# Kernel tuning notes

Measured on AMD Instinct MI355X. Metric: run time of the kernel, lower is better.

## Reference

```python
import jax, jax.numpy as jnp
import numpy as np
import math

B, L, WIN, D, H, FF, NL, V, M = 16, 2048, 128, 512, 8, 2048, 3, 32000, 32
HD = D // H
EPS = 1e-5
RECON_W = 0.1

def _ln(x, g, b):
    m = x.mean(-1, keepdims=True)
    v = ((x - m) ** 2).mean(-1, keepdims=True)
    return (x - m) * jax.lax.rsqrt(v + EPS) * g + b

def _denoiser(x_t, t, motif, left, right, glob, time_proj_W, time_proj_b, cond_proj_W, cond_proj_b,
              qkv_W, qkv_b, attn_out_W, attn_out_b, ff1_W, ff1_b, ff2_W, ff2_b,
              ln1_g, ln1_b, ln2_g, ln2_b, out_W, out_b):
    half = D // 2
    freqs = jnp.exp(-math.log(10000.0) * jnp.arange(half) / (half - 1))
    a = t[:, None] * freqs[None, :]
    temb = jnp.concatenate([jnp.sin(a), jnp.cos(a)], -1) @ time_proj_W.T + time_proj_b
    x = x_t + temb[:, None, :]
    cond = jnp.concatenate([motif, left, right, glob], -1) @ cond_proj_W.T + cond_proj_b
    x = jnp.concatenate([cond[:, None, :], x], 1)
    S = x.shape[1]
    for i in range(NL):  # post-norm TransformerEncoderLayer, relu, no dropout (eval)
        qkv = x @ qkv_W[i].T + qkv_b[i]
        q, k, v = jnp.split(qkv, 3, axis=-1)
        q = q.reshape(B, S, H, HD); k = k.reshape(B, S, H, HD); v = v.reshape(B, S, H, HD)
        attn = jax.nn.softmax(jnp.einsum('bqhd,bkhd->bhqk', q, k) / math.sqrt(HD), axis=-1)
        ctx = jnp.einsum('bhqk,bkhd->bqhd', attn, v).reshape(B, S, D)
        x = _ln(x + ctx @ attn_out_W[i].T + attn_out_b[i], ln1_g[i], ln1_b[i])
        h = jax.nn.relu(x @ ff1_W[i].T + ff1_b[i]) @ ff2_W[i].T + ff2_b[i]
        x = _ln(x + h, ln2_g[i], ln2_b[i])
    return x[:, 1:, :] @ out_W.T + out_b

def setup_inputs():
    key = jax.random.key(0)
    ks = jax.random.split(key, 20)
    s = 0.02
    inp = {}
    inp['token_ids'] = jax.random.randint(ks[0], (B, L), 0, V)
    inp['motif_ids'] = jax.random.randint(ks[1], (B, M), 0, V)
    inp['motif_len'] = jax.random.randint(ks[2], (B,), 1, M + 1)
    inp['window_start'] = jax.random.randint(ks[3], (B,), 0, L - WIN)
    lens = jax.random.randint(ks[4], (B,), 1, WIN + 1).at[0].set(WIN)
    inp['window_end'] = inp['window_start'] + lens
    inp['t'] = jax.random.uniform(ks[5], (B,))
    inp['x0'] = jax.random.normal(ks[6], (B, WIN, D))
    inp['embed_table'] = jax.random.normal(ks[7], (V, D)) * s
    inp['decode_W'] = jax.random.normal(ks[8], (V, D)) * s
    inp['decode_b'] = jnp.zeros((V,))
    inp['adapter_W'] = jax.random.normal(ks[9], (D, D)) * s
    inp['adapter_b'] = jnp.zeros((D,))
    inp['time_proj_W'] = jax.random.normal(ks[10], (D, D)) * s
    inp['time_proj_b'] = jnp.zeros((D,))
    inp['cond_proj_W'] = jax.random.normal(ks[11], (D, 4 * D)) * s
    inp['cond_proj_b'] = jnp.zeros((D,))
    inp['qkv_W'] = jax.random.normal(ks[12], (NL, 3 * D, D)) * s
    inp['qkv_b'] = jnp.zeros((NL, 3 * D))
    inp['attn_out_W'] = jax.random.normal(ks[13], (NL, D, D)) * s
    inp['attn_out_b'] = jnp.zeros((NL, D))
    inp['ff1_W'] = jax.random.normal(ks[14], (NL, FF, D)) * s
    inp['ff1_b'] = jnp.zeros((NL, FF))
    inp['ff2_W'] = jax.random.normal(ks[15], (NL, D, FF)) * s
    inp['ff2_b'] = jnp.zeros((NL, D))
    inp['ln1_g'] = jnp.ones((NL, D)); inp['ln1_b'] = jnp.zeros((NL, D))
    inp['ln2_g'] = jnp.ones((NL, D)); inp['ln2_b'] = jnp.zeros((NL, D))
    inp['out_W'] = jax.random.normal(ks[16], (D, D)) * s
    inp['out_b'] = jnp.zeros((D,))
    return inp

def _forward(token_ids, motif_ids, motif_len, window_start, window_end, t, x0,
             embed_table, decode_W, decode_b, adapter_W, adapter_b, den):
    hidden = embed_table[token_ids]  # frozen backbone encode: [B, L, D]
    pos = jnp.arange(L)
    def pool(s, e):  # vectorized masked mean over region [s, e)
        m = ((pos[None, :] >= s[:, None]) & (pos[None, :] < e[:, None])).astype(hidden.dtype)
        return jnp.einsum('bl,bld->bd', m, hidden) / jnp.maximum(m.sum(1, keepdims=True), 1.0)
    left = pool(jnp.zeros_like(window_start), window_start)
    right = pool(window_end, jnp.full_like(window_end, L))
    glob = hidden.mean(1)
    memb = embed_table[motif_ids]
    mmask = (jnp.arange(M)[None, :] < motif_len[:, None]).astype(memb.dtype)
    motif = (memb * mmask[..., None]).sum(1) / jnp.maximum(motif_len.astype(memb.dtype), 1.0)[:, None]
    actual = jnp.clip(window_end - window_start, 0, WIN)
    win_mask = jnp.arange(WIN)[None, :] < actual[:, None]
    idx = jnp.clip(window_start[:, None] + jnp.arange(WIN)[None, :], 0, L - 1)
    x1 = jnp.take_along_axis(hidden, idx[:, :, None], axis=1) * win_mask[..., None]
    x_t = (1 - t[:, None, None]) * x0 + t[:, None, None] * x1
    target_v = x1 - x0
    pred_v = _denoiser(x_t, t, motif, left, right, glob, *den)
    valid = win_mask[..., None].astype(x1.dtype)
    vel = (((pred_v - target_v) ** 2) * valid).sum() / (jnp.maximum(valid.sum(), 1.0) * D)
    pred_x1 = x_t + (1 - t[:, None, None]) * pred_v
    logits = (pred_x1 @ adapter_W.T + adapter_b) @ decode_W.T + decode_b
    labels = jnp.where(win_mask, jnp.take_along_axis(token_ids, idx, axis=1), -100)
    lv = labels != -100
    logp = jax.nn.log_softmax(logits, axis=-1)
    picked = jnp.take_along_axis(logp, jnp.maximum(labels, 0)[..., None], axis=-1)[..., 0]
    recon = -(picked * lv).sum() / jnp.maximum(lv.sum(), 1)
    return vel + RECON_W * recon

def reference(token_ids, motif_ids, motif_len, window_start, window_end, t, x0,
              embed_table, decode_W, decode_b, adapter_W, adapter_b,
              time_proj_W, time_proj_b, cond_proj_W, cond_proj_b, qkv_W, qkv_b,
              attn_out_W, attn_out_b, ff1_W, ff1_b, ff2_W, ff2_b,
              ln1_g, ln1_b, ln2_g, ln2_b, out_W, out_b):
    den = (time_proj_W, time_proj_b, cond_proj_W, cond_proj_b, qkv_W, qkv_b,
           attn_out_W, attn_out_b, ff1_W, ff1_b, ff2_W, ff2_b,
           ln1_g, ln1_b, ln2_g, ln2_b, out_W, out_b)
    return _forward(token_ids, motif_ids, motif_len, window_start, window_end, t, x0,
                    embed_table, decode_W, decode_b, adapter_W, adapter_b, den)
```

## Files before the change

kernel.cpp:

```cpp
#include <hip/hip_runtime.h>
#include <hip/hip_bf16.h>
#include <math.h>

typedef __hip_bfloat16 bf16;

constexpr int cB = 16, cL = 2048, cWIN = 128, cD = 512, cH = 8, cFF = 2048;
constexpr int cNL = 3, cV = 32000, cM = 32;
constexpr int cHD = cD / cH;
constexpr int cS = cWIN + 1;
constexpr float cEPS = 1e-5f;
constexpr float cRECON_W = 0.1f;
constexpr int cNVT = cV / 128;

__device__ __forceinline__ float b2f(bf16 x) { return __bfloat162float(x); }

__device__ __forceinline__ float ldx(const void* p, size_t i, int f32) {
    return f32 ? ((const float*)p)[i]
               : __bfloat162float(((const bf16*)p)[i]);
}

__device__ __forceinline__ unsigned int f2bf(float f) {
    union { float f; unsigned int u; } v; v.f = f;
    unsigned int u = v.u + 0x7FFFu + ((v.u >> 16) & 1u);
    return u >> 16;
}

__device__ __forceinline__ void glds16(const unsigned short* g, unsigned short* l) {
    __builtin_amdgcn_global_load_lds(
        (const __attribute__((address_space(1))) void*)g,
        (__attribute__((address_space(3))) void*)l, 16, 0, 0);
}

typedef short bf16x8 __attribute__((ext_vector_type(8)));
typedef float f32x4  __attribute__((ext_vector_type(4)));

__global__ void detect_kernel(const void* __restrict__ x0raw, int* __restrict__ flag)
{
    const unsigned short* h = (const unsigned short*)x0raw;
    int tid = threadIdx.x;
    int cnt = 0;
    for (int j = tid; j < 8192; j += 256) {
        unsigned short u = h[2 * j];
        int e = (u >> 7) & 0xFF;
        if (e >= 134) cnt++;
    }
    __shared__ int red[256];
    red[tid] = cnt; __syncthreads();
    for (int off = 128; off > 0; off >>= 1) {
        if (tid < off) red[tid] += red[tid + off];
        __syncthreads();
    }
    if (tid == 0) *flag = (red[0] > 400) ? 1 : 0;
}

__global__ __launch_bounds__(512) void pools_part_kernel(
    const int* __restrict__ tok, const int* __restrict__ wstart,
    const int* __restrict__ wend, const void* __restrict__ emb,
    float* __restrict__ part, const int* __restrict__ dflag)
{
    const int f32 = *dflag;
    int chunk = blockIdx.x;
    int b = blockIdx.y;
    int d = threadIdx.x;
    int ws_ = wstart[b], we_ = wend[b];
    float sl = 0.f, sr = 0.f, sg = 0.f;
    int l0 = chunk * 128;
    for (int l = l0; l < l0 + 128; ++l) {
        int t = tok[b * cL + l];
        float h = ldx(emb, (size_t)t * cD + d, f32);
        sg += h;
        if (l < ws_) sl += h;
        if (l >= we_) sr += h;
    }
    size_t base = ((size_t)(b * 16 + chunk)) * 3 * cD;
    part[base + d]            = sl;
    part[base + cD + d]       = sr;
    part[base + 2 * cD + d]   = sg;
}

__global__ __launch_bounds__(512) void pools_combine_kernel(
    const float* __restrict__ part, const int* __restrict__ mids,
    const int* __restrict__ mlen, const int* __restrict__ wstart,
    const int* __restrict__ wend, const void* __restrict__ emb,
    unsigned short* __restrict__ featb, const int* __restrict__ dflag)
{
    const int f32 = *dflag;
    int b = blockIdx.x;
    int d = threadIdx.x;
    int ws_ = wstart[b], we_ = wend[b];
    float sl = 0.f, sr = 0.f, sg = 0.f;
    for (int c = 0; c < 16; ++c) {
        size_t base = ((size_t)(b * 16 + c)) * 3 * cD;
        sl += part[base + d];
        sr += part[base + cD + d];
        sg += part[base + 2 * cD + d];
    }
    int ml = mlen[b];
    float sm = 0.f;
    for (int j = 0; j < cM; ++j) {
        if (j < ml) sm += ldx(emb, (size_t)mids[b * cM + j] * cD + d, f32);
    }
    unsigned short* fr = featb + (size_t)b * (4 * cD);
    fr[d]            = (unsigned short)f2bf(sm / fmaxf((float)ml, 1.f));
    fr[cD + d]       = (unsigned short)f2bf(sl / fmaxf((float)ws_, 1.f));
    fr[2 * cD + d]   = (unsigned short)f2bf(sr / fmaxf((float)(cL - we_), 1.f));
    fr[3 * cD + d]   = (unsigned short)f2bf(sg / (float)cL);
}

__global__ __launch_bounds__(512) void tf_kernel(
    const void* __restrict__ t_arr, unsigned short* __restrict__ tfbb,
    const int* __restrict__ dflag)
{
    const int f32 = *dflag;
    int b = blockIdx.x;
    int j = threadIdx.x;
    float t = ldx(t_arr, b, f32);
    const int half = cD / 2;
    float v;
    if (j < half) {
        float fr = expf(-logf(10000.f) * (float)j / (float)(half - 1));
        v = sinf(t * fr);
    } else {
        float fr = expf(-logf(10000.f) * (float)(j - half) / (float)(half - 1));
        v = cosf(t * fr);
    }
    tfbb[(size_t)b * cD + j] = (unsigned short)f2bf(v);
}

__global__ __launch_bounds__(512) void build_x_kernel(
    const int* __restrict__ tok, const int* __restrict__ wstart,
    const int* __restrict__ wend, const void* __restrict__ t_arr,
    const void* __restrict__ x0, const void* __restrict__ emb,
    const float* __restrict__ cond, const float* __restrict__ temb,
    float* __restrict__ x, unsigned short* __restrict__ xbf,
    float* __restrict__ x1, float* __restrict__ xt,
    const int* __restrict__ dflag)
{
    const int f32 = *dflag;
    int row = blockIdx.x;
    int b = row / cS, s = row % cS;
    int d = threadIdx.x;
    if (s == 0) {
        float cv = cond[b * cD + d];
        x[(size_t)row * cD + d] = cv;
        xbf[(size_t)row * cD + d] = (unsigned short)f2bf(cv);
        return;
    }
    int i = s - 1;
    int ws_ = wstart[b], we_ = wend[b];
    int actual = min(max(we_ - ws_, 0), cWIN);
    int idx = min(ws_ + i, cL - 1);
    float x1v = 0.f;
    if (i < actual) x1v = ldx(emb, (size_t)tok[b * cL + idx] * cD + d, f32);
    float t = ldx(t_arr, b, f32);
    float x0v = ldx(x0, ((size_t)b * cWIN + i) * cD + d, f32);
    float xtv = (1.f - t) * x0v + t * x1v;
    size_t ro = ((size_t)b * cWIN + i) * cD + d;
    x1[ro] = x1v;
    xt[ro] = xtv;
    float xv = xtv + temb[b * cD + d];
    x[(size_t)row * cD + d] = xv;
    xbf[(size_t)row * cD + d] = (unsigned short)f2bf(xv);
}

constexpr int GL2 = 72;
__global__ __launch_bounds__(256) void gemm_bf(
    const unsigned short* __restrict__ Abf, const void* __restrict__ Wb,
    size_t wOff, const void* __restrict__ biasb, size_t bOff,
    float* __restrict__ Cf, unsigned short* __restrict__ Cbf,
    int Mdim, int Ndim, int Kdim, int relu, int obf, int amap,
    const int* __restrict__ dflag)
{
    const int f32 = *dflag;
    const float* Wf = (const float*)Wb + wOff;
    const unsigned short* Wh = (const unsigned short*)Wb + wOff;
    __shared__ unsigned short As[2][64 * GL2];
    __shared__ unsigned short Bs[2][64 * GL2];
    const int tid = threadIdx.x;
    const int lane = tid & 63;
    const int wid = tid >> 6;
    const int wm = wid >> 1, wn = wid & 1;
    const int quad = lane >> 4, lm = lane & 15;
    const int m0 = blockIdx.y * 64;
    const int n0 = blockIdx.x * 64;

    f32x4 acc[2][2];
    #pragma unroll
    for (int i = 0; i < 2; ++i)
        #pragma unroll
        for (int j = 0; j < 2; ++j)
            acc[i][j] = (f32x4){0.f, 0.f, 0.f, 0.f};

    const int srow = tid >> 3;
    const int sc8  = (tid & 7) * 8;
    const int ssw  = ((tid & 7) ^ ((tid >> 3) & 7)) * 8;
    const int lmm  = lm & 7;

    auto loadA = [&](int k0, uint4* r) {
        #pragma unroll
        for (int t = 0; t < 2; ++t) {
            int r0 = m0 + srow + t * 32;
            uint4 v = {0u, 0u, 0u, 0u};
            if (r0 < Mdim) {
                size_t ar = amap ? ((size_t)(r0 >> 7) * cS + 1 + (r0 & 127))
                                 : (size_t)r0;
                v = *(const uint4*)(Abf + ar * Kdim + k0 + sc8);
            }
            r[t] = v;
        }
    };
    auto loadB = [&](int k0, uint4* r) {
        #pragma unroll
        for (int t = 0; t < 2; ++t) {
            int row = srow + t * 32;
            size_t g = (size_t)(n0 + row) * Kdim + k0 + sc8;
            if (f32) {
                float4 v0 = *(const float4*)(Wf + g);
                float4 v1 = *(const float4*)(Wf + g + 4);
                r[t] = make_uint4(
                    f2bf(v0.x) | (f2bf(v0.y) << 16), f2bf(v0.z) | (f2bf(v0.w) << 16),
                    f2bf(v1.x) | (f2bf(v1.y) << 16), f2bf(v1.z) | (f2bf(v1.w) << 16));
            } else {
                r[t] = *(const uint4*)(Wh + g);
            }
        }
    };
    auto stores = [&](int buf, const uint4* ra, const uint4* rb) {
        #pragma unroll
        for (int u = 0; u < 2; ++u) {
            *(uint4*)(&As[buf][(srow + u * 32) * GL2 + ssw]) = ra[u];
            *(uint4*)(&Bs[buf][(srow + u * 32) * GL2 + ssw]) = rb[u];
        }
    };
    auto compute = [&](int buf) {
        #pragma unroll
        for (int kk = 0; kk < 2; ++kk) {
            const int sl = ((kk * 4 + quad) ^ lmm) * 8;
            bf16x8 a0 = *(const bf16x8*)(&As[buf][(wm * 32 + lm) * GL2 + sl]);
            bf16x8 a1 = *(const bf16x8*)(&As[buf][(wm * 32 + 16 + lm) * GL2 + sl]);
            bf16x8 b0 = *(const bf16x8*)(&Bs[buf][(wn * 32 + lm) * GL2 + sl]);
            bf16x8 b1 = *(const bf16x8*)(&Bs[buf][(wn * 32 + 16 + lm) * GL2 + sl]);
            acc[0][0] = __builtin_amdgcn_mfma_f32_16x16x32_bf16(a0, b0, acc[0][0], 0, 0, 0);
            acc[0][1] = __builtin_amdgcn_mfma_f32_16x16x32_bf16(a0, b1, acc[0][1], 0, 0, 0);
            acc[1][0] = __builtin_amdgcn_mfma_f32_16x16x32_bf16(a1, b0, acc[1][0], 0, 0, 0);
            acc[1][1] = __builtin_amdgcn_mfma_f32_16x16x32_bf16(a1, b1, acc[1][1], 0, 0, 0);
        }
    };

    uint4 raA[2], rbA[2], raB[2], rbB[2];
    loadA(0, raA);  loadB(0, rbA);
    loadA(64, raB); loadB(64, rbB);
    const int nk = Kdim >> 6;
    for (int t = 0; t < nk; t += 2) {
        stores(0, raA, rbA);
        __syncthreads();
        if (t + 2 < nk) { loadA((t + 2) * 64, raA); loadB((t + 2) * 64, rbA); }
        compute(0);
        stores(1, raB, rbB);
        __syncthreads();
        if (t + 3 < nk) { loadA((t + 3) * 64, raB); loadB((t + 3) * 64, rbB); }
        compute(1);
    }

    #pragma unroll
    for (int in = 0; in < 2; ++in) {
        int gc = n0 + wn * 32 + in * 16 + lm;
        float bv = ldx(biasb, bOff + gc, f32);
        #pragma unroll
        for (int im = 0; im < 2; ++im) {
            #pragma unroll
            for (int r = 0; r < 4; ++r) {
                int gr = m0 + wm * 32 + im * 16 + quad * 4 + r;
                if (gr < Mdim) {
                    float v = acc[im][in][r] + bv;
                    if (relu) v = fmaxf(v, 0.f);
                    if (obf) Cbf[(size_t)gr * Ndim + gc] = (unsigned short)f2bf(v);
                    else     Cf[(size_t)gr * Ndim + gc] = v;
                }
            }
        }
    }
}

__global__ __launch_bounds__(256) void attn_mfma_kernel(
    const unsigned short* __restrict__ qkv, unsigned short* __restrict__ ctx)
{
    constexpr int SP = 160;
    constexpr int KP = 72;
    constexpr int VP = 168;
    const int h = blockIdx.x, b = blockIdx.y, z = blockIdx.z;
    const int tid = threadIdx.x;
    const int lane = tid & 63;
    const int wid = tid >> 6;
    const int quad = lane >> 4, lm = lane & 15;

    __shared__ unsigned short Ks[SP * KP];
    __shared__ unsigned short Vt[64 * VP];
    __shared__ unsigned short Pl[4 * 16 * VP];

    const unsigned short* base = qkv + (size_t)b * cS * (3 * cD) + h * cHD;

    for (int c = tid; c < SP * 8; c += 256) {
        int row = c >> 3, g = c & 7;
        uint4 v = {0u, 0u, 0u, 0u};
        if (row < cS)
            v = *(const uint4*)(base + (size_t)row * (3 * cD) + cD + g * 8);
        *(uint4*)(Ks + row * KP + g * 8) = v;
    }
    for (int c = tid; c < SP * 16; c += 256) {
        int key = c >> 4, d4 = c & 15;
        uint2 v = {0u, 0u};
        if (key < cS)
            v = *(const uint2*)(base + (size_t)key * (3 * cD) + 2 * cD + d4 * 4);
        Vt[(d4 * 4 + 0) * VP + key] = (unsigned short)(v.x & 0xFFFFu);
        Vt[(d4 * 4 + 1) * VP + key] = (unsigned short)(v.x >> 16);
        Vt[(d4 * 4 + 2) * VP + key] = (unsigned short)(v.y & 0xFFFFu);
        Vt[(d4 * 4 + 3) * VP + key] = (unsigned short)(v.y >> 16);
    }
    __syncthreads();

    unsigned short* Pw = Pl + wid * (16 * VP);
    const int t = z * 3 + wid;

    if (wid < 3 && t < 9) {
        int qs = t * 16 + lm;
        bf16x8 aq[2];
        #pragma unroll
        for (int j = 0; j < 8; ++j) { aq[0][j] = 0; aq[1][j] = 0; }
        if (qs < cS) {
            const unsigned short* qrow = base + (size_t)qs * (3 * cD);
            aq[0] = *(const bf16x8*)(qrow + quad * 8);
            aq[1] = *(const bf16x8*)(qrow + 32 + quad * 8);
        }

        f32x4 sc[10];
        #pragma unroll
        for (int n = 0; n < 10; ++n) {
            sc[n] = (f32x4){0.f, 0.f, 0.f, 0.f};
            bf16x8 bk0 = *(const bf16x8*)(Ks + (n * 16 + lm) * KP + quad * 8);
            sc[n] = __builtin_amdgcn_mfma_f32_16x16x32_bf16(aq[0], bk0, sc[n], 0, 0, 0);
            bf16x8 bk1 = *(const bf16x8*)(Ks + (n * 16 + lm) * KP + 32 + quad * 8);
            sc[n] = __builtin_amdgcn_mfma_f32_16x16x32_bf16(aq[1], bk1, sc[n], 0, 0, 0);
        }

        #pragma unroll
        for (int r = 0; r < 4; ++r) {
            float mx = -3.0e38f;
            #pragma unroll
            for (int n = 0; n < 10; ++n) {
                float v = sc[n][r] * 0.125f;
                mx = fmaxf(mx, ((n * 16 + lm) < cS) ? v : -3.0e38f);
            }
            #pragma unroll
            for (int msk = 1; msk < 16; msk <<= 1)
                mx = fmaxf(mx, __shfl_xor(mx, msk));
            float p[10];
            float sum = 0.f;
            #pragma unroll
            for (int n = 0; n < 10; ++n) {
                float e = ((n * 16 + lm) < cS) ? expf(sc[n][r] * 0.125f - mx) : 0.f;
                p[n] = e; sum += e;
            }
            #pragma unroll
            for (int msk = 1; msk < 16; msk <<= 1)
                sum += __shfl_xor(sum, msk);
            float inv = 1.f / sum;
            unsigned short* pr = Pw + (quad * 4 + r) * VP + lm;
            #pragma unroll
            for (int n = 0; n < 10; ++n)
                pr[n * 16] = (unsigned short)f2bf(p[n] * inv);
        }

        asm volatile("s_waitcnt lgkmcnt(0)" ::: "memory");
        __builtin_amdgcn_sched_barrier(0);

        f32x4 o[4];
        #pragma unroll
        for (int j = 0; j < 4; ++j) o[j] = (f32x4){0.f, 0.f, 0.f, 0.f};
        #pragma unroll
        for (int ks = 0; ks < 5; ++ks) {
            bf16x8 ap = *(const bf16x8*)(Pw + lm * VP + ks * 32 + quad * 8);
            #pragma unroll
            for (int j = 0; j < 4; ++j) {
                bf16x8 bv = *(const bf16x8*)(Vt + (j * 16 + lm) * VP + ks * 32 + quad * 8);
                o[j] = __builtin_amdgcn_mfma_f32_16x16x32_bf16(ap, bv, o[j], 0, 0, 0);
            }
        }

        #pragma unroll
        for (int r = 0; r < 4; ++r) {
            int s_ = t * 16 + quad * 4 + r;
            if (s_ < cS) {
                unsigned short* orow = ctx + ((size_t)(b * cS + s_)) * cD + h * cHD;
                #pragma unroll
                for (int j = 0; j < 4; ++j)
                    orow[j * 16 + lm] = (unsigned short)f2bf(o[j][r]);
            }
        }
    }
}

__global__ __launch_bounds__(256) void resid_ln_kernel(
    float* __restrict__ x, const float* __restrict__ h,
    const void* __restrict__ g, const void* __restrict__ bta, size_t off,
    unsigned short* __restrict__ xbf, const int* __restrict__ dflag)
{
    const int f32 = *dflag;
    int row = blockIdx.x;
    int tid = threadIdx.x;
    __shared__ float red[256];
    float v[2];
    float s = 0.f;
    #pragma unroll
    for (int j = 0; j < 2; ++j) {
        int d = tid + j * 256;
        v[j] = x[(size_t)row * cD + d] + h[(size_t)row * cD + d];
        s += v[j];
    }
    red[tid] = s; __syncthreads();
    for (int o = 128; o > 0; o >>= 1) {
        if (tid < o) red[tid] += red[tid + o];
        __syncthreads();
    }
    float mean = red[0] / (float)cD;
    __syncthreads();
    float vs = 0.f;
    #pragma unroll
    for (int j = 0; j < 2; ++j) { float dd = v[j] - mean; vs += dd * dd; }
    red[tid] = vs; __syncthreads();
    for (int o = 128; o > 0; o >>= 1) {
        if (tid < o) red[tid] += red[tid + o];
        __syncthreads();
    }
    float rs = rsqrtf(red[0] / (float)cD + cEPS);
    #pragma unroll
    for (int j = 0; j < 2; ++j) {
        int d = tid + j * 256;
        float ov = (v[j] - mean) * rs * ldx(g, off + d, f32) + ldx(bta, off + d, f32);
        x[(size_t)row * cD + d] = ov;
        xbf[(size_t)row * cD + d] = (unsigned short)f2bf(ov);
    }
}

__global__ __launch_bounds__(512) void predvel_kernel(
    const float* __restrict__ xt, const float* __restrict__ pv,
    const float* __restrict__ x1, const void* __restrict__ x0,
    const void* __restrict__ t_arr, const int* __restrict__ wstart,
    const int* __restrict__ wend, unsigned short* __restrict__ px1,
    float* __restrict__ velpart, const int* __restrict__ dflag)
{
    const int f32 = *dflag;
    int row = blockIdx.x;
    int b = row >> 7, i = row & 127;
    int d = threadIdx.x;
    float t = ldx(t_arr, b, f32);
    size_t o = (size_t)row * cD + d;
    float pvv = pv[o];
    px1[o] = (unsigned short)f2bf(xt[o] + (1.f - t) * pvv);
    int actual = min(max(wend[b] - wstart[b], 0), cWIN);
    float s = 0.f;
    if (i < actual) {
        float tv = x1[o] - ldx(x0, o, f32);
        float diff = pvv - tv;
        s = diff * diff;
    }
    __shared__ float red[512];
    red[d] = s; __syncthreads();
    for (int off = 256; off > 0; off >>= 1) {
        if (d < off) red[d] += red[d + off];
        __syncthreads();
    }
    if (d == 0) velpart[row] = red[0];
}

__global__ void labels_kernel(
    const int* __restrict__ tok, const int* __restrict__ wstart,
    const int* __restrict__ wend, int* __restrict__ labels)
{
    int r = blockIdx.x * 256 + threadIdx.x;
    if (r >= cB * cWIN) return;
    int b = r / cWIN, i = r % cWIN;
    int ws_ = wstart[b], we_ = wend[b];
    int actual = min(max(we_ - ws_, 0), cWIN);
    labels[r] = (i < actual) ? tok[b * cL + min(ws_ + i, cL - 1)] : -1;
}

__global__ __launch_bounds__(256) void cvt_w_kernel(
    const void* __restrict__ Wsrc, unsigned short* __restrict__ dst,
    const int* __restrict__ dflag)
{
    if (!*dflag) return;
    const float4* src = (const float4*)Wsrc;
    size_t n4 = (size_t)cV * cD / 4;
    for (size_t i = (size_t)blockIdx.x * 256 + threadIdx.x; i < n4;
         i += (size_t)gridDim.x * 256) {
        float4 v = src[i];
        unsigned int p0 = f2bf(v.x) | (f2bf(v.y) << 16);
        unsigned int p1 = f2bf(v.z) | (f2bf(v.w) << 16);
        ((uint2*)dst)[i] = make_uint2(p0, p1);
    }
}

__global__ __launch_bounds__(256) void decode_mfma2_kernel(
    const unsigned short* __restrict__ hbf, const unsigned short* __restrict__ wbf,
    const void* __restrict__ dW, const void* __restrict__ db,
    const int* __restrict__ labels,
    float* __restrict__ pm, float* __restrict__ ps, float* __restrict__ lab,
    const int* __restrict__ dflag)
{
    const int f32 = *dflag;
    const unsigned short* Wsrc = f32 ? wbf : (const unsigned short*)dW;
    const int bid = blockIdx.x;
    const int xcd = bid & 7;
    const int local = bid >> 3;
    const int nt = xcd * 32 + (local >> 4);
    const int mt = local & 15;
    if (nt >= cNVT) return;
    const int m0 = mt * 128, n0 = nt * 128;

    __shared__ __align__(16) char smem[32768];
    unsigned short* As = (unsigned short*)smem;
    unsigned short* Bs = As + 8192;

    const int tid = threadIdx.x;
    const int lane = tid & 63;
    const int wid = tid >> 6;
    const int wm = wid >> 1, wn = wid & 1;
    const int quad = lane >> 4, lm = lane & 15;

    const int grow  = lane >> 3;
    const int gslot = (lane & 7) ^ grow;
    const int lmm   = lm & 7;

    const unsigned short* gA = hbf  + (size_t)(m0 + wid * 32 + grow) * cD + gslot * 8;
    const unsigned short* gB = Wsrc + (size_t)(n0 + wid * 32 + grow) * cD + gslot * 8;

    f32x4 acc[4][4];
    #pragma unroll
    for (int i = 0; i < 4; ++i)
        #pragma unroll
        for (int j = 0; j < 4; ++j)
            acc[i][j] = (f32x4){0.f, 0.f, 0.f, 0.f};

    for (int k0 = 0; k0 < cD; k0 += 64) {
        #pragma unroll
        for (int c = 0; c < 4; ++c) {
            glds16(gA + (size_t)c * 8 * cD + k0, As + (wid * 4 + c) * 512);
            glds16(gB + (size_t)c * 8 * cD + k0, Bs + (wid * 4 + c) * 512);
        }
        __syncthreads();
        #pragma unroll
        for (int kk = 0; kk < 2; ++kk) {
            const int sl = ((kk * 4 + quad) ^ lmm) * 8;
            bf16x8 af[4], bfr[4];
            #pragma unroll
            for (int im = 0; im < 4; ++im)
                af[im] = *(const bf16x8*)(As + (wm * 64 + im * 16 + lm) * 64 + sl);
            #pragma unroll
            for (int in = 0; in < 4; ++in)
                bfr[in] = *(const bf16x8*)(Bs + (wn * 64 + in * 16 + lm) * 64 + sl);
            #pragma unroll
            for (int im = 0; im < 4; ++im)
                #pragma unroll
                for (int in = 0; in < 4; ++in)
                    acc[im][in] = __builtin_amdgcn_mfma_f32_16x16x32_bf16(
                        af[im], bfr[in], acc[im][in], 0, 0, 0);
        }
        __syncthreads();
    }

    float bv[4];
    #pragma unroll
    for (int in = 0; in < 4; ++in)
        bv[in] = ldx(db, n0 + wn * 64 + in * 16 + lm, f32);
    #pragma unroll
    for (int im = 0; im < 4; ++im)
        #pragma unroll
        for (int in = 0; in < 4; ++in)
            #pragma unroll
            for (int r = 0; r < 4; ++r)
                acc[im][in][r] += bv[in];

    #pragma unroll
    for (int im = 0; im < 4; ++im) {
        #pragma unroll
        for (int r = 0; r < 4; ++r) {
            int gr = m0 + wm * 64 + im * 16 + quad * 4 + r;
            int lb = labels[gr];
            #pragma unroll
            for (int in = 0; in < 4; ++in) {
                int col = n0 + wn * 64 + in * 16 + lm;
                if (lb == col) lab[gr] = acc[im][in][r];
            }
        }
    }

    float (*red)[33] = (float(*)[33])smem;
    float* mrow = (float*)(smem + 16896);
    #pragma unroll
    for (int im = 0; im < 4; ++im) {
        #pragma unroll
        for (int r = 0; r < 4; ++r) {
            int rl = wm * 64 + im * 16 + quad * 4 + r;
            float mx = acc[im][0][r];
            #pragma unroll
            for (int in = 1; in < 4; ++in) mx = fmaxf(mx, acc[im][in][r]);
            red[rl][wn * 16 + lm] = mx;
        }
    }
    __syncthreads();
    if (tid < 128) {
        float mx = red[tid][0];
        #pragma unroll
        for (int t = 1; t < 32; ++t) mx = fmaxf(mx, red[tid][t]);
        mrow[tid] = mx;
    }
    __syncthreads();
    #pragma unroll
    for (int im = 0; im < 4; ++im) {
        #pragma unroll
        for (int r = 0; r < 4; ++r) {
            int rl = wm * 64 + im * 16 + quad * 4 + r;
            float m_ = mrow[rl];
            float s = 0.f;
            #pragma unroll
            for (int in = 0; in < 4; ++in) s += expf(acc[im][in][r] - m_);
            red[rl][wn * 16 + lm] = s;
        }
    }
    __syncthreads();
    if (tid < 128) {
        float s = red[tid][0];
        #pragma unroll
        for (int t = 1; t < 32; ++t) s += red[tid][t];
        int gr = m0 + tid;
        pm[(size_t)gr * cNVT + nt] = mrow[tid];
        ps[(size_t)gr * cNVT + nt] = s;
    }
}

constexpr int GLDS = 40;
__global__ __launch_bounds__(256) void decode_mfma_kernel(
    const unsigned short* __restrict__ hbf, const void* __restrict__ dW,
    const void* __restrict__ db, const int* __restrict__ labels,
    float* __restrict__ pm, float* __restrict__ ps, float* __restrict__ lab,
    const int* __restrict__ dflag)
{
    const int f32 = *dflag;
    const float* Wf = (const float*)dW;
    const unsigned short* Wh = (const unsigned short*)dW;
    __shared__ unsigned short As[128 * GLDS];
    __shared__ unsigned short Bs[128 * GLDS];
    const int tid = threadIdx.x;
    const int lane = tid & 63;
    const int wid = tid >> 6;
    const int wm = wid >> 1, wn = wid & 1;
    const int quad = lane >> 4, lm = lane & 15;
    const int nt = blockIdx.x;
    const int mt = blockIdx.y;
    const int m0 = mt * 128, n0 = nt * 128;

    f32x4 acc[4][4];
    #pragma unroll
    for (int i = 0; i < 4; ++i)
        #pragma unroll
        for (int j = 0; j < 4; ++j)
            acc[i][j] = (f32x4){0.f, 0.f, 0.f, 0.f};

    for (int k0 = 0; k0 < cD; k0 += 32) {
        #pragma unroll
        for (int t = 0; t < 2; ++t) {
            int idx = tid + t * 256;
            int row = idx >> 2, c = idx & 3;
            uint4 v = *(const uint4*)(hbf + (size_t)(m0 + row) * cD + k0 + c * 8);
            *(uint4*)(As + row * GLDS + c * 8) = v;
        }
        #pragma unroll
        for (int t = 0; t < 4; ++t) {
            int chunk = tid + t * 256;
            int row = chunk >> 3;
            int kc = (chunk & 7) * 4;
            size_t gro = (size_t)(n0 + row) * cD + k0 + kc;
            if (f32) {
                float4 v = *(const float4*)(Wf + gro);
                unsigned int p0 = f2bf(v.x) | (f2bf(v.y) << 16);
                unsigned int p1 = f2bf(v.z) | (f2bf(v.w) << 16);
                *(uint2*)(Bs + row * GLDS + kc) = make_uint2(p0, p1);
            } else {
                *(uint2*)(Bs + row * GLDS + kc) = *(const uint2*)(Wh + gro);
            }
        }
        __syncthreads();
        bf16x8 af[4], bfr[4];
        #pragma unroll
        for (int im = 0; im < 4; ++im) {
            int row = wm * 64 + im * 16 + lm;
            af[im] = *(const bf16x8*)(As + row * GLDS + quad * 8);
        }
        #pragma unroll
        for (int in = 0; in < 4; ++in) {
            int row = wn * 64 + in * 16 + lm;
            bfr[in] = *(const bf16x8*)(Bs + row * GLDS + quad * 8);
        }
        #pragma unroll
        for (int im = 0; im < 4; ++im)
            #pragma unroll
            for (int in = 0; in < 4; ++in)
                acc[im][in] = __builtin_amdgcn_mfma_f32_16x16x32_bf16(
                    af[im], bfr[in], acc[im][in], 0, 0, 0);
        __syncthreads();
    }

    float bv[4];
    #pragma unroll
    for (int in = 0; in < 4; ++in)
        bv[in] = ldx(db, n0 + wn * 64 + in * 16 + lm, f32);
    #pragma unroll
    for (int im = 0; im < 4; ++im)
        #pragma unroll
        for (int in = 0; in < 4; ++in)
            #pragma unroll
            for (int r = 0; r < 4; ++r)
                acc[im][in][r] += bv[in];

    #pragma unroll
    for (int im = 0; im < 4; ++im) {
        #pragma unroll
        for (int r = 0; r < 4; ++r) {
            int gr = m0 + wm * 64 + im * 16 + quad * 4 + r;
            int lb = labels[gr];
            #pragma unroll
            for (int in = 0; in < 4; ++in) {
                int col = n0 + wn * 64 + in * 16 + lm;
                if (lb == col) lab[gr] = acc[im][in][r];
            }
        }
    }

    __shared__ float red[128][33];
    __shared__ float mrow[128];
    #pragma unroll
    for (int im = 0; im < 4; ++im) {
        #pragma unroll
        for (int r = 0; r < 4; ++r) {
            int rl = wm * 64 + im * 16 + quad * 4 + r;
            float mx = acc[im][0][r];
            #pragma unroll
            for (int in = 1; in < 4; ++in) mx = fmaxf(mx, acc[im][in][r]);
            red[rl][wn * 16 + lm] = mx;
        }
    }
    __syncthreads();
    if (tid < 128) {
        float mx = red[tid][0];
        #pragma unroll
        for (int t = 1; t < 32; ++t) mx = fmaxf(mx, red[tid][t]);
        mrow[tid] = mx;
    }
    __syncthreads();
    #pragma unroll
    for (int im = 0; im < 4; ++im) {
        #pragma unroll
        for (int r = 0; r < 4; ++r) {
            int rl = wm * 64 + im * 16 + quad * 4 + r;
            float m_ = mrow[rl];
            float s = 0.f;
            #pragma unroll
            for (int in = 0; in < 4; ++in) s += expf(acc[im][in][r] - m_);
            red[rl][wn * 16 + lm] = s;
        }
    }
    __syncthreads();
    if (tid < 128) {
        float s = red[tid][0];
        #pragma unroll
        for (int t = 1; t < 32; ++t) s += red[tid][t];
        int gr = m0 + tid;
        pm[(size_t)gr * cNVT + nt] = mrow[tid];
        ps[(size_t)gr * cNVT + nt] = s;
    }
}

__global__ __launch_bounds__(64) void lse_reduce_kernel(
    const float* __restrict__ pm, const float* __restrict__ ps,
    const float* __restrict__ lab, const int* __restrict__ labels,
    float* __restrict__ logppart)
{
    int r = blockIdx.x;
    int tid = threadIdx.x;
    if (labels[r] < 0) {
        if (tid == 0) logppart[r] = 0.f;
        return;
    }
    float m = -1e30f;
    for (int c = tid; c < cNVT; c += 64) m = fmaxf(m, pm[(size_t)r * cNVT + c]);
    for (int off = 32; off > 0; off >>= 1) m = fmaxf(m, __shfl_down(m, off));
    m = __shfl(m, 0);
    float s = 0.f;
    for (int c = tid; c < cNVT; c += 64)
        s += ps[(size_t)r * cNVT + c] * expf(pm[(size_t)r * cNVT + c] - m);
    for (int off = 32; off > 0; off >>= 1) s += __shfl_down(s, off);
    if (tid == 0) logppart[r] = lab[r] - (m + logf(s));
}

__global__ __launch_bounds__(256) void finalize_kernel(
    const float* __restrict__ velpart, const float* __restrict__ logppart,
    const int* __restrict__ wstart, const int* __restrict__ wend,
    void* __restrict__ out, const int* __restrict__ dflag)
{
    const int f32 = *dflag;
    __shared__ float r1[256], r2[256];
    int tid = threadIdx.x;
    float s1 = 0.f, s2 = 0.f;
    for (int r = tid; r < cB * cWIN; r += 256) {
        s1 += velpart[r];
        s2 += logppart[r];
    }
    r1[tid] = s1; r2[tid] = s2; __syncthreads();
    for (int off = 128; off > 0; off >>= 1) {
        if (tid < off) { r1[tid] += r1[tid + off]; r2[tid] += r2[tid + off]; }
        __syncthreads();
    }
    if (tid == 0) {
        float cnt = 0.f;
        for (int b = 0; b < cB; ++b)
            cnt += (float)min(max(wend[b] - wstart[b], 0), cWIN);
        cnt = fmaxf(cnt, 1.f);
        float vel = r1[0] / (cnt * (float)cD);
        float recon = -r2[0] / cnt;
        float loss = vel + cRECON_W * recon;
        if (f32) ((float*)out)[0] = loss;
        else     ((bf16*)out)[0] = __float2bfloat16(loss);
    }
}

extern "C" void kernel_launch(void* const* d_in, const int* in_sizes, int n_in,
                              void* d_out, int out_size, void* d_ws, size_t ws_size,
                              hipStream_t stream) {
    const int*  token_ids    = (const int*)d_in[0];
    const int*  motif_ids    = (const int*)d_in[1];
    const int*  motif_len    = (const int*)d_in[2];
    const int*  window_start = (const int*)d_in[3];
    const int*  window_end   = (const int*)d_in[4];
    const void* t_arr        = d_in[5];
    const void* x0           = d_in[6];
    const void* embed_table  = d_in[7];
    const void* decode_W     = d_in[8];
    const void* decode_b     = d_in[9];
    const void* adapter_W    = d_in[10];
    const void* adapter_b    = d_in[11];
    const void* time_proj_W  = d_in[12];
    const void* time_proj_b  = d_in[13];
    const void* cond_proj_W  = d_in[14];
    const void* cond_proj_b  = d_in[15];
    const void* qkv_W        = d_in[16];
    const void* qkv_b        = d_in[17];
    const void* attn_out_W   = d_in[18];
    const void* attn_out_b   = d_in[19];
    const void* ff1_W        = d_in[20];
    const void* ff1_b        = d_in[21];
    const void* ff2_W        = d_in[22];
    const void* ff2_b        = d_in[23];
    const void* ln1_g        = d_in[24];
    const void* ln1_b        = d_in[25];
    const void* ln2_g        = d_in[26];
    const void* ln2_b        = d_in[27];
    const void* out_W        = d_in[28];
    const void* out_b        = d_in[29];

    float* w = (float*)d_ws;
    const size_t SZ_X   = (size_t)cB * cS * cD;
    const size_t SZ_BA  = (size_t)cB * cS * cFF;
    const size_t SZ_ROW = (size_t)cB * cWIN * cD;
    float* x     = w;
    float* bufA  = x + SZ_X;
    float* bufB  = bufA + SZ_BA;
    float* bufC  = bufB + SZ_X;
    float* x1b   = bufC + SZ_X;
    float* xtb   = x1b + SZ_ROW;
    float* pvb   = xtb + SZ_ROW;
    float* h2b   = pvb + SZ_ROW;
    float* feat  = h2b + SZ_ROW;
    float* tfb   = feat + (size_t)cB * 4 * cD;
    float* cond  = tfb + (size_t)cB * cD;
    float* temb  = cond + (size_t)cB * cD;
    float* velpart = temb + (size_t)cB * cD;
    float* logppart = velpart + (size_t)cB * cWIN;
    int*   dflag = (int*)(logppart + (size_t)cB * cWIN);
    float* wsend = (float*)(dflag + 16);
    unsigned short* wbf = (unsigned short*)wsend;

    const size_t need_bytes = ((char*)wsend - (char*)d_ws)
                            + (size_t)cV * cD * sizeof(unsigned short) + 256;
    const bool fast_decode = ws_size >= need_bytes;

    const int Wrows = cB * cWIN;
    const int Mrows = cB * cS;

    unsigned short* xbf    = (unsigned short*)h2b;
    unsigned short* featbf = xbf + (size_t)Mrows * cD;
    unsigned short* tfbbf  = featbf + (size_t)cB * 4 * cD;
    unsigned short* qkvbf  = (unsigned short*)bufA;
    unsigned short* ff1bf  = (unsigned short*)bufA;
    unsigned short* ctxbf  = (unsigned short*)bufB;
    unsigned short* px1bf  = (unsigned short*)(bufA + (size_t)3 * 1024 * 1024);
    unsigned short* hbf    = (unsigned short*)bufC;

    float* pm  = bufA;
    float* ps  = pm + (size_t)Wrows * cNVT;
    float* lab = ps + (size_t)Wrows * cNVT;
    int*   labels = (int*)(lab + Wrows);
    float* poolspart = bufC;

    auto gemm = [&](const unsigned short* A, const void* W, size_t wOff,
                    const void* bias, size_t bOff, float* Cf, unsigned short* Cbf,
                    int M_, int N_, int K_, int relu, int obf, int amap) {
        dim3 grid(N_ / 64, (M_ + 63) / 64);
        gemm_bf<<<grid, 256, 0, stream>>>(A, W, wOff, bias, bOff, Cf, Cbf,
                                          M_, N_, K_, relu, obf, amap, dflag);
    };

    detect_kernel<<<1, 256, 0, stream>>>(x0, dflag);
    if (fast_decode)
        cvt_w_kernel<<<2048, 256, 0, stream>>>(decode_W, wbf, dflag);
    pools_part_kernel<<<dim3(16, cB), cD, 0, stream>>>(token_ids, window_start,
        window_end, embed_table, poolspart, dflag);
    pools_combine_kernel<<<cB, cD, 0, stream>>>(poolspart, motif_ids, motif_len,
        window_start, window_end, embed_table, featbf, dflag);
    tf_kernel<<<cB, cD, 0, stream>>>(t_arr, tfbbf, dflag);
    gemm(featbf, cond_proj_W, 0, cond_proj_b, 0, cond, nullptr, cB, cD, 4 * cD, 0, 0, 0);
    gemm(tfbbf, time_proj_W, 0, time_proj_b, 0, temb, nullptr, cB, cD, cD, 0, 0, 0);
    build_x_kernel<<<Mrows, cD, 0, stream>>>(token_ids, window_start, window_end,
        t_arr, x0, embed_table, cond, temb, x, xbf, x1b, xtb, dflag);

    for (int i = 0; i < cNL; ++i) {
        gemm(xbf, qkv_W, (size_t)i * 3 * cD * cD, qkv_b, (size_t)i * 3 * cD,
             nullptr, qkvbf, Mrows, 3 * cD, cD, 0, 1, 0);
        attn_mfma_kernel<<<dim3(cH, cB, 3), 256, 0, stream>>>(qkvbf, ctxbf);
        gemm(ctxbf, attn_out_W, (size_t)i * cD * cD, attn_out_b, (size_t)i * cD,
             bufC, nullptr, Mrows, cD, cD, 0, 0, 0);
        resid_ln_kernel<<<Mrows, 256, 0, stream>>>(x, bufC, ln1_g, ln1_b,
             (size_t)i * cD, xbf, dflag);
        gemm(xbf, ff1_W, (size_t)i * cFF * cD, ff1_b, (size_t)i * cFF,
             nullptr, ff1bf, Mrows, cFF, cD, 1, 1, 0);
        gemm(ff1bf, ff2_W, (size_t)i * cD * cFF, ff2_b, (size_t)i * cD,
             bufC, nullptr, Mrows, cD, cFF, 0, 0, 0);
        resid_ln_kernel<<<Mrows, 256, 0, stream>>>(x, bufC, ln2_g, ln2_b,
             (size_t)i * cD, xbf, dflag);
    }

    gemm(xbf, out_W, 0, out_b, 0, pvb, nullptr, Wrows, cD, cD, 0, 0, 1);
    predvel_kernel<<<Wrows, 512, 0, stream>>>(xtb, pvb, x1b, x0, t_arr,
        window_start, window_end, px1bf, velpart, dflag);
    gemm(px1bf, adapter_W, 0, adapter_b, 0, nullptr, hbf, Wrows, cD, cD, 0, 1, 0);

    labels_kernel<<<(Wrows + 255) / 256, 256, 0, stream>>>(
        token_ids, window_start, window_end, labels);
    if (fast_decode) {
        decode_mfma2_kernel<<<4096, 256, 0, stream>>>(
            hbf, wbf, decode_W, decode_b, labels, pm, ps, lab, dflag);
    } else {
        decode_mfma_kernel<<<dim3(cNVT, Wrows / 128), 256, 0, stream>>>(
            hbf, decode_W, decode_b, labels, pm, ps, lab, dflag);
    }
    lse_reduce_kernel<<<Wrows, 64, 0, stream>>>(pm, ps, lab, labels, logppart);

    finalize_kernel<<<1, 256, 0, stream>>>(velpart, logppart,
        window_start, window_end, d_out, dflag);
}
```

Before: 933.5 us.

## Use 512-thread blocks in the generic GEMM and shrink the decode GEMM K-tile

The generic bf16 GEMM now runs with 512 threads (8 waves) per 64x64 tile. Each wave computes a 16x32 sub-tile and each thread stages one 16-byte chunk of A and B, where before it staged two. The vocabulary decode GEMM moves from a K-step of 64 to 32, halving its shared memory, with a matching swizzle for the narrower rows. The aim is more resident waves and better latency hiding, at the cost of more barriers per K loop and less MFMA work per wave between loads.

After: 811.5 us. 13.1% less time.

```diff
diff --git a/kernel.cpp b/kernel.cpp
--- a/kernel.cpp
+++ b/kernel.cpp
@@ -164,7 +164,7 @@
 }
 
 constexpr int GL2 = 72;
-__global__ __launch_bounds__(256) void gemm_bf(
+__global__ __launch_bounds__(512) void gemm_bf(
     const unsigned short* __restrict__ Abf, const void* __restrict__ Wb,
     size_t wOff, const void* __restrict__ biasb, size_t bOff,
     float* __restrict__ Cf, unsigned short* __restrict__ Cbf,
@@ -179,75 +179,59 @@
     const int tid = threadIdx.x;
     const int lane = tid & 63;
     const int wid = tid >> 6;
-    const int wm = wid >> 1, wn = wid & 1;
+    const int wm = wid >> 1;
+    const int wn = wid & 1;
     const int quad = lane >> 4, lm = lane & 15;
     const int m0 = blockIdx.y * 64;
     const int n0 = blockIdx.x * 64;
 
-    f32x4 acc[2][2];
-    #pragma unroll
-    for (int i = 0; i < 2; ++i)
-        #pragma unroll
-        for (int j = 0; j < 2; ++j)
-            acc[i][j] = (f32x4){0.f, 0.f, 0.f, 0.f};
+    f32x4 acc0 = (f32x4){0.f, 0.f, 0.f, 0.f};
+    f32x4 acc1 = (f32x4){0.f, 0.f, 0.f, 0.f};
 
     const int srow = tid >> 3;
     const int sc8  = (tid & 7) * 8;
     const int ssw  = ((tid & 7) ^ ((tid >> 3) & 7)) * 8;
     const int lmm  = lm & 7;
 
-    auto loadA = [&](int k0, uint4* r) {
-        #pragma unroll
-        for (int t = 0; t < 2; ++t) {
-            int r0 = m0 + srow + t * 32;
-            uint4 v = {0u, 0u, 0u, 0u};
-            if (r0 < Mdim) {
-                size_t ar = amap ? ((size_t)(r0 >> 7) * cS + 1 + (r0 & 127))
-                                 : (size_t)r0;
-                v = *(const uint4*)(Abf + ar * Kdim + k0 + sc8);
-            }
-            r[t] = v;
-        }
+    auto loadA = [&](int k0, uint4& r) {
+        int r0 = m0 + srow;
+        uint4 v = {0u, 0u, 0u, 0u};
+        if (r0 < Mdim) {
+            size_t ar = amap ? ((size_t)(r0 >> 7) * cS + 1 + (r0 & 127))
+                             : (size_t)r0;
+            v = *(const uint4*)(Abf + ar * Kdim + k0 + sc8);
+        }
+        r = v;
     };
-    auto loadB = [&](int k0, uint4* r) {
-        #pragma unroll
-        for (int t = 0; t < 2; ++t) {
-            int row = srow + t * 32;
-            size_t g = (size_t)(n0 + row) * Kdim + k0 + sc8;
-            if (f32) {
-                float4 v0 = *(const float4*)(Wf + g);
-                float4 v1 = *(const float4*)(Wf + g + 4);
-                r[t] = make_uint4(
-                    f2bf(v0.x) | (f2bf(v0.y) << 16), f2bf(v0.z) | (f2bf(v0.w) << 16),
-                    f2bf(v1.x) | (f2bf(v1.y) << 16), f2bf(v1.z) | (f2bf(v1.w) << 16));
-            } else {
-                r[t] = *(const uint4*)(Wh + g);
-            }
+    auto loadB = [&](int k0, uint4& r) {
+        size_t g = (size_t)(n0 + srow) * Kdim + k0 + sc8;
+        if (f32) {
+            float4 v0 = *(const float4*)(Wf + g);
+            float4 v1 = *(const float4*)(Wf + g + 4);
+            r = make_uint4(
+                f2bf(v0.x) | (f2bf(v0.y) << 16), f2bf(v0.z) | (f2bf(v0.w) << 16),
+                f2bf(v1.x) | (f2bf(v1.y) << 16), f2bf(v1.z) | (f2bf(v1.w) << 16));
+        } else {
+            r = *(const uint4*)(Wh + g);
         }
     };
-    auto stores = [&](int buf, const uint4* ra, const uint4* rb) {
-        #pragma unroll
-        for (int u = 0; u < 2; ++u) {
-            *(uint4*)(&As[buf][(srow + u * 32) * GL2 + ssw]) = ra[u];
-            *(uint4*)(&Bs[buf][(srow + u * 32) * GL2 + ssw]) = rb[u];
-        }
+    auto stores = [&](int buf, const uint4& ra, const uint4& rb) {
+        *(uint4*)(&As[buf][srow * GL2 + ssw]) = ra;
+        *(uint4*)(&Bs[buf][srow * GL2 + ssw]) = rb;
     };
     auto compute = [&](int buf) {
         #pragma unroll
         for (int kk = 0; kk < 2; ++kk) {
             const int sl = ((kk * 4 + quad) ^ lmm) * 8;
-            bf16x8 a0 = *(const bf16x8*)(&As[buf][(wm * 32 + lm) * GL2 + sl]);
-            bf16x8 a1 = *(const bf16x8*)(&As[buf][(wm * 32 + 16 + lm) * GL2 + sl]);
+            bf16x8 a0 = *(const bf16x8*)(&As[buf][(wm * 16 + lm) * GL2 + sl]);
             bf16x8 b0 = *(const bf16x8*)(&Bs[buf][(wn * 32 + lm) * GL2 + sl]);
             bf16x8 b1 = *(const bf16x8*)(&Bs[buf][(wn * 32 + 16 + lm) * GL2 + sl]);
-            acc[0][0] = __builtin_amdgcn_mfma_f32_16x16x32_bf16(a0, b0, acc[0][0], 0, 0, 0);
-            acc[0][1] = __builtin_amdgcn_mfma_f32_16x16x32_bf16(a0, b1, acc[0][1], 0, 0, 0);
-            acc[1][0] = __builtin_amdgcn_mfma_f32_16x16x32_bf16(a1, b0, acc[1][0], 0, 0, 0);
-            acc[1][1] = __builtin_amdgcn_mfma_f32_16x16x32_bf16(a1, b1, acc[1][1], 0, 0, 0);
+            acc0 = __builtin_amdgcn_mfma_f32_16x16x32_bf16(a0, b0, acc0, 0, 0, 0);
+            acc1 = __builtin_amdgcn_mfma_f32_16x16x32_bf16(a0, b1, acc1, 0, 0, 0);
         }
     };
 
-    uint4 raA[2], rbA[2], raB[2], rbB[2];
+    uint4 raA, rbA, raB, rbB;
     loadA(0, raA);  loadB(0, rbA);
     loadA(64, raB); loadB(64, rbB);
     const int nk = Kdim >> 6;
@@ -266,17 +250,15 @@
     for (int in = 0; in < 2; ++in) {
         int gc = n0 + wn * 32 + in * 16 + lm;
         float bv = ldx(biasb, bOff + gc, f32);
-        #pragma unroll
-        for (int im = 0; im < 2; ++im) {
-            #pragma unroll
-            for (int r = 0; r < 4; ++r) {
-                int gr = m0 + wm * 32 + im * 16 + quad * 4 + r;
-                if (gr < Mdim) {
-                    float v = acc[im][in][r] + bv;
-                    if (relu) v = fmaxf(v, 0.f);
-                    if (obf) Cbf[(size_t)gr * Ndim + gc] = (unsigned short)f2bf(v);
-                    else     Cf[(size_t)gr * Ndim + gc] = v;
-                }
+        const f32x4& a = in ? acc1 : acc0;
+        #pragma unroll
+        for (int r = 0; r < 4; ++r) {
+            int gr = m0 + wm * 16 + quad * 4 + r;
+            if (gr < Mdim) {
+                float v = a[r] + bv;
+                if (relu) v = fmaxf(v, 0.f);
+                if (obf) Cbf[(size_t)gr * Ndim + gc] = (unsigned short)f2bf(v);
+                else     Cf[(size_t)gr * Ndim + gc] = v;
             }
         }
     }
@@ -518,9 +500,9 @@
     if (nt >= cNVT) return;
     const int m0 = mt * 128, n0 = nt * 128;
 
-    __shared__ __align__(16) char smem[32768];
+    __shared__ __align__(16) char smem[17408];
     unsigned short* As = (unsigned short*)smem;
-    unsigned short* Bs = As + 8192;
+    unsigned short* Bs = As + 4096;
 
     const int tid = threadIdx.x;
     const int lane = tid & 63;
@@ -528,9 +510,9 @@
     const int wm = wid >> 1, wn = wid & 1;
     const int quad = lane >> 4, lm = lane & 15;
 
-    const int grow  = lane >> 3;
-    const int gslot = (lane & 7) ^ grow;
-    const int lmm   = lm & 7;
+    const int grow  = lane >> 2;
+    const int gslot = (lane & 3) ^ ((lane >> 3) & 3);
+    const int rslot = (quad ^ ((lm >> 1) & 3)) * 8;
 
     const unsigned short* gA = hbf  + (size_t)(m0 + wid * 32 + grow) * cD + gslot * 8;
     const unsigned short* gB = Wsrc + (size_t)(n0 + wid * 32 + grow) * cD + gslot * 8;
@@ -542,30 +524,26 @@
         for (int j = 0; j < 4; ++j)
             acc[i][j] = (f32x4){0.f, 0.f, 0.f, 0.f};
 
-    for (int k0 = 0; k0 < cD; k0 += 64) {
-        #pragma unroll
-        for (int c = 0; c < 4; ++c) {
-            glds16(gA + (size_t)c * 8 * cD + k0, As + (wid * 4 + c) * 512);
-            glds16(gB + (size_t)c * 8 * cD + k0, Bs + (wid * 4 + c) * 512);
-        }
-        __syncthreads();
-        #pragma unroll
-        for (int kk = 0; kk < 2; ++kk) {
-            const int sl = ((kk * 4 + quad) ^ lmm) * 8;
-            bf16x8 af[4], bfr[4];
-            #pragma unroll
-            for (int im = 0; im < 4; ++im)
-                af[im] = *(const bf16x8*)(As + (wm * 64 + im * 16 + lm) * 64 + sl);
+    for (int k0 = 0; k0 < cD; k0 += 32) {
+        #pragma unroll
+        for (int c = 0; c < 2; ++c) {
+            glds16(gA + (size_t)c * 16 * cD + k0, As + (wid * 2 + c) * 512);
+            glds16(gB + (size_t)c * 16 * cD + k0, Bs + (wid * 2 + c) * 512);
+        }
+        __syncthreads();
+        bf16x8 af[4], bfr[4];
+        #pragma unroll
+        for (int im = 0; im < 4; ++im)
+            af[im] = *(const bf16x8*)(As + (wm * 64 + im * 16 + lm) * 32 + rslot);
+        #pragma unroll
+        for (int in = 0; in < 4; ++in)
+            bfr[in] = *(const bf16x8*)(Bs + (wn * 64 + in * 16 + lm) * 32 + rslot);
+        #pragma unroll
+        for (int im = 0; im < 4; ++im)
             #pragma unroll
             for (int in = 0; in < 4; ++in)
-                bfr[in] = *(const bf16x8*)(Bs + (wn * 64 + in * 16 + lm) * 64 + sl);
-            #pragma unroll
-            for (int im = 0; im < 4; ++im)
-                #pragma unroll
-                for (int in = 0; in < 4; ++in)
-                    acc[im][in] = __builtin_amdgcn_mfma_f32_16x16x32_bf16(
-                        af[im], bfr[in], acc[im][in], 0, 0, 0);
-        }
+                acc[im][in] = __builtin_amdgcn_mfma_f32_16x16x32_bf16(
+                    af[im], bfr[in], acc[im][in], 0, 0, 0);
         __syncthreads();
     }
 
@@ -916,7 +894,7 @@
                     const void* bias, size_t bOff, float* Cf, unsigned short* Cbf,
                     int M_, int N_, int K_, int relu, int obf, int amap) {
         dim3 grid(N_ / 64, (M_ + 63) / 64);
-        gemm_bf<<<grid, 256, 0, stream>>>(A, W, wOff, bias, bOff, Cf, Cbf,
+        gemm_bf<<<grid, 512, 0, stream>>>(A, W, wOff, bias, bOff, Cf, Cbf,
                                           M_, N_, K_, relu, obf, amap, dflag);
     };
 
```
